# Performance work log

Measured on AMD Instinct MI355X. Metric: run time of the kernel, lower is better.

Reference implementation:

```python
import jax, jax.numpy as jnp
import numpy as np

B, S, D, H = 2, 2048, 1024, 16
DK = D // H

def setup_inputs() -> dict:
    key = jax.random.key(0)
    ks = jax.random.split(key, 5)
    scale = 1.0 / np.sqrt(D)
    return {
        "x": jax.random.normal(ks[0], (B, S, D), dtype=jnp.float32),
        "W_qkv": jax.random.uniform(ks[1], (D, 3 * D), dtype=jnp.float32, minval=-scale, maxval=scale),
        "b_qkv": jax.random.uniform(ks[2], (3 * D,), dtype=jnp.float32, minval=-scale, maxval=scale),
        "W_o": jax.random.uniform(ks[3], (D, D), dtype=jnp.float32, minval=-scale, maxval=scale),
        "b_o": jax.random.uniform(ks[4], (D,), dtype=jnp.float32, minval=-scale, maxval=scale),
    }

def reference(x, W_qkv, b_qkv, W_o, b_o):
    # fused QKV projection: [B,S,3D] -> [B,S,H,3*dk]
    qkv = (x @ W_qkv + b_qkv).reshape(B, S, H, 3 * DK)
    q, k, v = qkv[..., :DK], qkv[..., DK:2 * DK], qkv[..., 2 * DK:]
    # scores [B,H,S,S]; note: original module's masked_fill is a discarded no-op, so no mask applied
    a = jnp.einsum("bqhd,bkhd->bhqk", q, k) / np.sqrt(DK).astype(np.float32)
    a = jax.nn.softmax(a, axis=-1)
    o = jnp.einsum("bhqk,bkhd->bqhd", a, v).reshape(B, S, D)
    return o @ W_o + b_o
```

## Files before the change

kernel.cpp:

```cpp
#include <hip/hip_runtime.h>
#include <hip/hip_bf16.h>

typedef __bf16 bf16;
typedef __attribute__((ext_vector_type(8))) __bf16 bf16x8;
typedef __attribute__((ext_vector_type(4))) __bf16 bf16x4;
typedef __attribute__((ext_vector_type(4))) float f32x4;
typedef __attribute__((ext_vector_type(16))) float f32x16;
typedef __attribute__((ext_vector_type(4))) unsigned int u32x4;
typedef __attribute__((ext_vector_type(2))) unsigned int u32x2;

#define DEV static __device__ __forceinline__

DEV f32x4 mfma16(bf16x8 a, bf16x8 b, f32x4 c) {
  return __builtin_amdgcn_mfma_f32_16x16x32_bf16(a, b, c, 0, 0, 0);
}
DEV f32x16 mfma32(bf16x8 a, bf16x8 b, f32x16 c) {
  return __builtin_amdgcn_mfma_f32_32x32x16_bf16(a, b, c, 0, 0, 0);
}
DEV unsigned int pk2(float a, float b) {
  unsigned short ua = __builtin_bit_cast(unsigned short, (bf16)a);
  unsigned short ub = __builtin_bit_cast(unsigned short, (bf16)b);
  return ((unsigned int)ub << 16) | ua;
}
DEV void gload16(const void* g, void* l) {
  __builtin_amdgcn_global_load_lds(
      (const __attribute__((address_space(1))) unsigned int*)g,
      (__attribute__((address_space(3))) unsigned int*)l, 16, 0, 0);
}
DEV u32x2 xhalf(unsigned int a, unsigned int b, int hi) {
#if __has_builtin(__builtin_amdgcn_permlane32_swap)
  return __builtin_amdgcn_permlane32_swap(a, b, false, false);
#else
  unsigned int xa = __shfl_xor(a, 32), xb = __shfl_xor(b, 32);
  u32x2 r;
  r.x = hi ? xb : a;
  r.y = hi ? b : xa;
  return r;
#endif
}


__global__ __launch_bounds__(256) void xbf_k(const float* __restrict__ x,
                                             bf16* __restrict__ xb) {
  int gid = blockIdx.x * 256 + threadIdx.x;
  const float* src = x + (size_t)gid * 8;
  f32x4 a0 = *(const f32x4*)src;
  f32x4 a1 = *(const f32x4*)(src + 4);
  bf16x8 pk;
#pragma unroll
  for (int j = 0; j < 4; ++j) { pk[j] = (bf16)a0[j]; pk[j + 4] = (bf16)a1[j]; }
  *(bf16x8*)(xb + (size_t)gid * 8) = pk;
}

__global__ __launch_bounds__(256) void wt_k(const float* __restrict__ w,
                                            bf16* __restrict__ wt, int N, int K) {
  __shared__ bf16 ts[64][68];
  const int tid = threadIdx.x;
  const int n0 = blockIdx.x * 64, k0 = blockIdx.y * 64;
  const int tr = tid >> 4;
  const int tc = (tid & 15) * 4;
#pragma unroll
  for (int p = 0; p < 4; ++p) {
    int kr = p * 16 + tr;
    f32x4 v = *(const f32x4*)(w + (size_t)(k0 + kr) * N + n0 + tc);
#pragma unroll
    for (int j = 0; j < 4; ++j) ts[tc + j][kr] = (bf16)v[j];
  }
  __syncthreads();
#pragma unroll
  for (int p = 0; p < 4; ++p) {
    int nr = p * 16 + tr;
    bf16x4 o4;
#pragma unroll
    for (int j = 0; j < 4; ++j) o4[j] = ts[nr][tc + j];
    *(bf16x4*)(wt + (size_t)(n0 + nr) * K + k0 + tc) = o4;
  }
}

__global__ __launch_bounds__(256, 2) void qkv_gemm_k(
    const bf16* __restrict__ xb, const bf16* __restrict__ wt,
    const float* __restrict__ bias,
    bf16* __restrict__ qo, bf16* __restrict__ ko, bf16* __restrict__ vt) {
  __shared__ __align__(16) char As[16384];
  __shared__ __align__(16) char Bs[16384];
  const int tid = threadIdx.x;
  const int lane = tid & 63;
  const int wid = tid >> 6;
  const int wm = wid >> 1, wn = wid & 1;
  const int l16 = lane & 15, lhi = lane >> 4;
  const int m0 = blockIdx.y * 128;
  const int n0 = blockIdx.x * 128;
  const char* ap = (const char*)xb;
  const char* bp = (const char*)wt;

  f32x4 acc[4][4] = {};

  for (int kt = 0; kt < 1024; kt += 64) {
#pragma unroll
    for (int i = 0; i < 4; ++i) {
      int n = i * 256 + wid * 64 + lane;
      int row = n >> 3, c16 = n & 7;
      gload16(ap + (size_t)(m0 + row) * 2048 + kt * 2 + ((c16 * 16) ^ ((row & 7) << 4)),
              As + (i * 256 + wid * 64) * 16);
    }
#pragma unroll
    for (int i = 0; i < 4; ++i) {
      int n = i * 256 + wid * 64 + lane;
      int row = n >> 3, c16 = n & 7;
      gload16(bp + (size_t)(n0 + row) * 2048 + kt * 2 + ((c16 * 16) ^ ((row & 7) << 4)),
              Bs + (i * 256 + wid * 64) * 16);
    }
    __syncthreads();
#pragma unroll
    for (int kc = 0; kc < 2; ++kc) {
      bf16x8 af[4], bfr[4];
#pragma unroll
      for (int ii = 0; ii < 4; ++ii) {
        int row = wm * 64 + ii * 16 + l16;
        af[ii] = *(const bf16x8*)(As + row * 128 +
                                  ((kc * 64 + lhi * 16) ^ ((row & 7) << 4)));
      }
#pragma unroll
      for (int jj = 0; jj < 4; ++jj) {
        int n = wn * 64 + jj * 16 + l16;
        bfr[jj] = *(const bf16x8*)(Bs + n * 128 +
                                   ((kc * 64 + lhi * 16) ^ ((n & 7) << 4)));
      }
#pragma unroll
      for (int ii = 0; ii < 4; ++ii)
#pragma unroll
        for (int jj = 0; jj < 4; ++jj)
          acc[ii][jj] = mfma16(af[ii], bfr[jj], acc[ii][jj]);
    }
    __syncthreads();
  }

  const float SCQ = 0.18033688011112042f;
#pragma unroll
  for (int jj = 0; jj < 4; ++jj) {
    int nbase = n0 + wn * 64 + jj * 16;
    int h = nbase / 192;
    int rem = nbase - h * 192;
    int type = rem >> 6;
    int dk0 = rem & 63;
    float bv = bias[nbase + l16];
    if (type < 2) {
      bf16* dst = (type == 0) ? qo : ko;
      float scl = (type == 0) ? SCQ : 1.0f;
#pragma unroll
      for (int ii = 0; ii < 4; ++ii) {
#pragma unroll
        for (int r = 0; r < 4; ++r) {
          int mrow = m0 + wm * 64 + ii * 16 + lhi * 4 + r;
          int b = mrow >> 11, s = mrow & 2047;
          dst[(size_t)((b * 16 + h) * 2048 + s) * 64 + dk0 + l16] =
              (bf16)((acc[ii][jj][r] + bv) * scl);
        }
      }
    } else {
#pragma unroll
      for (int ii = 0; ii < 4; ++ii) {
        int s0 = m0 + wm * 64 + ii * 16 + lhi * 4;
        int b = s0 >> 11, s = s0 & 2047;
        bf16x4 w4;
#pragma unroll
        for (int r = 0; r < 4; ++r) w4[r] = (bf16)(acc[ii][jj][r] + bv);
        *(bf16x4*)(vt + (size_t)((b * 16 + h) * 64 + dk0 + l16) * 2048 + s) = w4;
      }
    }
  }
}

__global__ __launch_bounds__(256, 4) void attn_k(
    const bf16* __restrict__ q, const bf16* __restrict__ k,
    const bf16* __restrict__ vt, float* __restrict__ opart,
    float* __restrict__ lpart) {
  __shared__ __align__(16) char Ks[2][8192];
  __shared__ __align__(16) char Vs[2][8192];
  const int tid = threadIdx.x;
  const int lane = tid & 63;
  const int wid = tid >> 6;
  const int l31 = lane & 31;
  const int hi = lane >> 5;
  const int bh = blockIdx.x;
  const int half = blockIdx.z;
  const bf16* qp = q + (size_t)bh * 2048 * 64;
  const char* kp = (const char*)(k + (size_t)bh * 2048 * 64);
  const char* vp = (const char*)(vt + (size_t)bh * 64 * 2048);
  const int q0 = blockIdx.y * 128 + wid * 32;
  const int kv0 = half * 1024;

  bf16x8 qf[4];
#pragma unroll
  for (int c = 0; c < 4; ++c)
    qf[c] = *(const bf16x8*)(qp + (size_t)(q0 + l31) * 64 + c * 16 + 8 * hi);

  f32x16 ot0 = {}, ot1 = {};
  float l_ = 0.f;

  auto STAGE = [&](int kt, int bs) {
#pragma unroll
    for (int i = 0; i < 2; ++i) {
      int n = i * 256 + wid * 64 + lane;
      int row = n >> 3, c16 = n & 7;
      const char* src = kp + (size_t)(kt + row) * 128 + ((c16 * 16) ^ ((row & 7) << 4));
      gload16(src, Ks[bs] + (i * 256 + wid * 64) * 16);
    }
#pragma unroll
    for (int i = 0; i < 2; ++i) {
      int n = i * 256 + wid * 64 + lane;
      int row = n >> 3, c16 = n & 7;
      const char* src = vp + (size_t)row * 4096 + (size_t)kt * 2 +
                        ((c16 * 16) ^ ((row & 7) << 4));
      gload16(src, Vs[bs] + (i * 256 + wid * 64) * 16);
    }
  };

  STAGE(kv0, 0);
  __syncthreads();

  for (int t = 0; t < 16; ++t) {
    int bs = t & 1;
    if (t < 15) STAGE(kv0 + (t + 1) * 64, bs ^ 1);

    float p[2][16];
#pragma unroll
    for (int kb = 0; kb < 2; ++kb) {
      bf16x8 kf[4];
#pragma unroll
      for (int c = 0; c < 4; ++c) {
        int row = kb * 32 + l31;
        kf[c] = *(const bf16x8*)(Ks[bs] + row * 128 +
                                 ((c * 32 + 16 * hi) ^ ((row & 7) << 4)));
      }
      f32x16 st = {};
      __builtin_amdgcn_s_setprio(1);
#pragma unroll
      for (int c = 0; c < 4; ++c) st = mfma32(kf[c], qf[c], st);
      __builtin_amdgcn_s_setprio(0);
#pragma unroll
      for (int r = 0; r < 16; ++r) {
        p[kb][r] = __builtin_amdgcn_exp2f(st[r]);
        l_ += p[kb][r];
      }
    }

#pragma unroll
    for (int ch = 0; ch < 4; ++ch) {
      const int kb = ch >> 1, off = (ch & 1) * 8;
      unsigned int w0 = pk2(p[kb][off + 0], p[kb][off + 1]);
      unsigned int w1 = pk2(p[kb][off + 2], p[kb][off + 3]);
      unsigned int w2 = pk2(p[kb][off + 4], p[kb][off + 5]);
      unsigned int w3 = pk2(p[kb][off + 6], p[kb][off + 7]);
      u32x2 s02 = xhalf(w0, w2, hi);
      u32x2 s13 = xhalf(w1, w3, hi);
      u32x4 ww;
      ww.x = s02.x;
      ww.y = s13.x;
      ww.z = s02.y;
      ww.w = s13.y;
      bf16x8 pb = __builtin_bit_cast(bf16x8, ww);
      int r0 = l31, r1 = 32 + l31;
      bf16x8 vf0 = *(const bf16x8*)(Vs[bs] + r0 * 128 +
                                    ((ch * 32 + 16 * hi) ^ ((r0 & 7) << 4)));
      bf16x8 vf1 = *(const bf16x8*)(Vs[bs] + r1 * 128 +
                                    ((ch * 32 + 16 * hi) ^ ((r1 & 7) << 4)));
      __builtin_amdgcn_s_setprio(1);
      ot0 = mfma32(vf0, pb, ot0);
      ot1 = mfma32(vf1, pb, ot1);
      __builtin_amdgcn_s_setprio(0);
    }
    __syncthreads();
  }

  float ltot = l_ + __shfl_xor(l_, 32);
  if (hi == 0) lpart[(size_t)(half * 32 + bh) * 2048 + q0 + l31] = ltot;

  float* op = opart + ((size_t)(half * 32 + bh) * 2048 + q0 + l31) * 64;
#pragma unroll
  for (int g = 0; g < 4; ++g) {
    f32x4 a4, b4;
#pragma unroll
    for (int j = 0; j < 4; ++j) { a4[j] = ot0[g * 4 + j]; b4[j] = ot1[g * 4 + j]; }
    *(f32x4*)(op + 8 * g + 4 * hi) = a4;
    *(f32x4*)(op + 32 + 8 * g + 4 * hi) = b4;
  }
}

__global__ __launch_bounds__(256) void comb_k(const float* __restrict__ opart,
                                              const float* __restrict__ lpart,
                                              bf16* __restrict__ o) {
  const size_t HS = 32ull * 2048 * 64;
  int gid = blockIdx.x * 256 + threadIdx.x;
  int dq = gid & 15;
  int s = (gid >> 4) & 2047;
  int bh = gid >> 15;
  size_t i0 = ((size_t)bh * 2048 + s) * 64 + dq * 4;
  f32x4 a = *(const f32x4*)(opart + i0);
  f32x4 b2 = *(const f32x4*)(opart + HS + i0);
  float l0 = lpart[(size_t)bh * 2048 + s];
  float l1 = lpart[32ull * 2048 + (size_t)bh * 2048 + s];
  float inv = 1.f / (l0 + l1);
  int b = bh >> 4, h = bh & 15;
  bf16x4 r;
#pragma unroll
  for (int j = 0; j < 4; ++j) r[j] = (bf16)((a[j] + b2[j]) * inv);
  *(bf16x4*)(o + (size_t)(b * 2048 + s) * 1024 + h * 64 + dq * 4) = r;
}

__global__ __launch_bounds__(256, 2) void out_gemm_k(
    const bf16* __restrict__ a, const bf16* __restrict__ wt,
    const float* __restrict__ bias, float* __restrict__ out) {
  __shared__ __align__(16) char As[16384];
  __shared__ __align__(16) char Bs[16384];
  const int tid = threadIdx.x;
  const int lane = tid & 63;
  const int wid = tid >> 6;
  const int wm = wid >> 1, wn = wid & 1;
  const int l16 = lane & 15, lhi = lane >> 4;
  const int m0 = blockIdx.y * 128;
  const int n0 = blockIdx.x * 128;
  const char* ap = (const char*)a;
  const char* bp = (const char*)wt;

  f32x4 acc[4][4] = {};

  for (int kt = 0; kt < 1024; kt += 64) {
#pragma unroll
    for (int i = 0; i < 4; ++i) {
      int n = i * 256 + wid * 64 + lane;
      int row = n >> 3, c16 = n & 7;
      gload16(ap + (size_t)(m0 + row) * 2048 + kt * 2 + ((c16 * 16) ^ ((row & 7) << 4)),
              As + (i * 256 + wid * 64) * 16);
    }
#pragma unroll
    for (int i = 0; i < 4; ++i) {
      int n = i * 256 + wid * 64 + lane;
      int row = n >> 3, c16 = n & 7;
      gload16(bp + (size_t)(n0 + row) * 2048 + kt * 2 + ((c16 * 16) ^ ((row & 7) << 4)),
              Bs + (i * 256 + wid * 64) * 16);
    }
    __syncthreads();
#pragma unroll
    for (int kc = 0; kc < 2; ++kc) {
      bf16x8 af[4], bfr[4];
#pragma unroll
      for (int ii = 0; ii < 4; ++ii) {
        int row = wm * 64 + ii * 16 + l16;
        af[ii] = *(const bf16x8*)(As + row * 128 +
                                  ((kc * 64 + lhi * 16) ^ ((row & 7) << 4)));
      }
#pragma unroll
      for (int jj = 0; jj < 4; ++jj) {
        int n = wn * 64 + jj * 16 + l16;
        bfr[jj] = *(const bf16x8*)(Bs + n * 128 +
                                   ((kc * 64 + lhi * 16) ^ ((n & 7) << 4)));
      }
#pragma unroll
      for (int ii = 0; ii < 4; ++ii)
#pragma unroll
        for (int jj = 0; jj < 4; ++jj)
          acc[ii][jj] = mfma16(af[ii], bfr[jj], acc[ii][jj]);
    }
    __syncthreads();
  }

#pragma unroll
  for (int jj = 0; jj < 4; ++jj) {
    int nbase = n0 + wn * 64 + jj * 16;
    float bv = bias[nbase + l16];
#pragma unroll
    for (int ii = 0; ii < 4; ++ii) {
#pragma unroll
      for (int r = 0; r < 4; ++r) {
        int mrow = m0 + wm * 64 + ii * 16 + lhi * 4 + r;
        out[(size_t)mrow * 1024 + nbase + l16] = acc[ii][jj][r] + bv;
      }
    }
  }
}

extern "C" void kernel_launch(void* const* d_in, const int* in_sizes, int n_in,
                              void* d_out, int out_size, void* d_ws, size_t ws_size,
                              hipStream_t stream) {
  const float* x = (const float*)d_in[0];
  const float* wqkv = (const float*)d_in[1];
  const float* bqkv = (const float*)d_in[2];
  const float* wo = (const float*)d_in[3];
  const float* bo = (const float*)d_in[4];
  float* out = (float*)d_out;

  bf16* qws = (bf16*)d_ws;
  bf16* kws = qws + 4194304;
  bf16* vtws = kws + 4194304;
  bf16* ows = vtws + 4194304;
  bf16* wqkvT = ows + 4194304;
  bf16* woT = wqkvT + 3145728;
  float* opart = (float*)(woT + 1048576);
  float* lpart = opart + 8388608;
  bf16* xbf = (bf16*)opart;

  xbf_k<<<2048, 256, 0, stream>>>(x, xbf);
  wt_k<<<dim3(48, 16), 256, 0, stream>>>(wqkv, wqkvT, 3072, 1024);
  wt_k<<<dim3(16, 16), 256, 0, stream>>>(wo, woT, 1024, 1024);
  qkv_gemm_k<<<dim3(24, 32), 256, 0, stream>>>(xbf, wqkvT, bqkv, qws, kws, vtws);
  attn_k<<<dim3(32, 16, 2), 256, 0, stream>>>(qws, kws, vtws, opart, lpart);
  comb_k<<<4096, 256, 0, stream>>>(opart, lpart, ows);
  out_gemm_k<<<dim3(8, 32), 256, 0, stream>>>(ows, woT, bo, out);
}
```

Before: 129.2 us.

## Double query rows per attention wave and merge prep kernels into one launch

Each attention wave now handles 64 query rows instead of 32, so every K/V fragment read from LDS feeds twice as many MFMAs. The grid shrinks to 512 blocks and launch bounds drop to 2 blocks per SIMD group to make room for the larger register footprint. Separately, the x bf16 conversion and the two weight transposes are folded into a single launch to save launch overhead. The cost is fewer resident waves and fewer blocks, which reduces latency hiding and parallelism on a 256-CU device.

```diff
diff --git a/kernel.cpp b/kernel.cpp
--- a/kernel.cpp
+++ b/kernel.cpp
@@ -40,23 +40,36 @@
 }
 
 
-__global__ __launch_bounds__(256) void xbf_k(const float* __restrict__ x,
-                                             bf16* __restrict__ xb) {
-  int gid = blockIdx.x * 256 + threadIdx.x;
-  const float* src = x + (size_t)gid * 8;
-  f32x4 a0 = *(const f32x4*)src;
-  f32x4 a1 = *(const f32x4*)(src + 4);
-  bf16x8 pk;
-#pragma unroll
-  for (int j = 0; j < 4; ++j) { pk[j] = (bf16)a0[j]; pk[j + 4] = (bf16)a1[j]; }
-  *(bf16x8*)(xb + (size_t)gid * 8) = pk;
-}
-
-__global__ __launch_bounds__(256) void wt_k(const float* __restrict__ w,
-                                            bf16* __restrict__ wt, int N, int K) {
+__global__ __launch_bounds__(256) void prep_k(
+    const float* __restrict__ x, bf16* __restrict__ xb,
+    const float* __restrict__ wqkv, bf16* __restrict__ wqkvT,
+    const float* __restrict__ wo, bf16* __restrict__ woT) {
   __shared__ bf16 ts[64][68];
   const int tid = threadIdx.x;
-  const int n0 = blockIdx.x * 64, k0 = blockIdx.y * 64;
+  const int bid = blockIdx.x;
+  if (bid < 2048) {
+    int gid = bid * 256 + tid;
+    const float* src = x + (size_t)gid * 8;
+    f32x4 a0 = *(const f32x4*)src;
+    f32x4 a1 = *(const f32x4*)(src + 4);
+    bf16x8 pk;
+#pragma unroll
+    for (int j = 0; j < 4; ++j) { pk[j] = (bf16)a0[j]; pk[j + 4] = (bf16)a1[j]; }
+    *(bf16x8*)(xb + (size_t)gid * 8) = pk;
+    return;
+  }
+  const float* w;
+  bf16* wt;
+  int N, K, n0, k0;
+  if (bid < 2816) {
+    int r = bid - 2048;
+    w = wqkv; wt = wqkvT; N = 3072; K = 1024;
+    n0 = (r % 48) * 64; k0 = (r / 48) * 64;
+  } else {
+    int r = bid - 2816;
+    w = wo; wt = woT; N = 1024; K = 1024;
+    n0 = (r % 16) * 64; k0 = (r / 16) * 64;
+  }
   const int tr = tid >> 4;
   const int tc = (tid & 15) * 4;
 #pragma unroll
@@ -171,7 +184,7 @@
   }
 }
 
-__global__ __launch_bounds__(256, 4) void attn_k(
+__global__ __launch_bounds__(256, 2) void attn_k(
     const bf16* __restrict__ q, const bf16* __restrict__ k,
     const bf16* __restrict__ vt, float* __restrict__ opart,
     float* __restrict__ lpart) {
@@ -187,16 +200,18 @@
   const bf16* qp = q + (size_t)bh * 2048 * 64;
   const char* kp = (const char*)(k + (size_t)bh * 2048 * 64);
   const char* vp = (const char*)(vt + (size_t)bh * 64 * 2048);
-  const int q0 = blockIdx.y * 128 + wid * 32;
+  const int q0 = blockIdx.y * 256 + wid * 64;
   const int kv0 = half * 1024;
 
-  bf16x8 qf[4];
-#pragma unroll
-  for (int c = 0; c < 4; ++c)
-    qf[c] = *(const bf16x8*)(qp + (size_t)(q0 + l31) * 64 + c * 16 + 8 * hi);
-
-  f32x16 ot0 = {}, ot1 = {};
-  float l_ = 0.f;
+  bf16x8 qf0[4], qf1[4];
+#pragma unroll
+  for (int c = 0; c < 4; ++c) {
+    qf0[c] = *(const bf16x8*)(qp + (size_t)(q0 + l31) * 64 + c * 16 + 8 * hi);
+    qf1[c] = *(const bf16x8*)(qp + (size_t)(q0 + 32 + l31) * 64 + c * 16 + 8 * hi);
+  }
+
+  f32x16 ot00 = {}, ot01 = {}, ot10 = {}, ot11 = {};
+  float l0 = 0.f, l1 = 0.f;
 
   auto STAGE = [&](int kt, int bs) {
 #pragma unroll
@@ -223,7 +238,6 @@
     int bs = t & 1;
     if (t < 15) STAGE(kv0 + (t + 1) * 64, bs ^ 1);
 
-    float p[2][16];
 #pragma unroll
     for (int kb = 0; kb < 2; ++kb) {
       bf16x8 kf[4];
@@ -233,57 +247,83 @@
         kf[c] = *(const bf16x8*)(Ks[bs] + row * 128 +
                                  ((c * 32 + 16 * hi) ^ ((row & 7) << 4)));
       }
-      f32x16 st = {};
+      f32x16 st0 = {}, st1 = {};
       __builtin_amdgcn_s_setprio(1);
 #pragma unroll
-      for (int c = 0; c < 4; ++c) st = mfma32(kf[c], qf[c], st);
+      for (int c = 0; c < 4; ++c) {
+        st0 = mfma32(kf[c], qf0[c], st0);
+        st1 = mfma32(kf[c], qf1[c], st1);
+      }
       __builtin_amdgcn_s_setprio(0);
+      float p0[16], p1[16];
 #pragma unroll
       for (int r = 0; r < 16; ++r) {
-        p[kb][r] = __builtin_amdgcn_exp2f(st[r]);
-        l_ += p[kb][r];
-      }
-    }
-
-#pragma unroll
-    for (int ch = 0; ch < 4; ++ch) {
-      const int kb = ch >> 1, off = (ch & 1) * 8;
-      unsigned int w0 = pk2(p[kb][off + 0], p[kb][off + 1]);
-      unsigned int w1 = pk2(p[kb][off + 2], p[kb][off + 3]);
-      unsigned int w2 = pk2(p[kb][off + 4], p[kb][off + 5]);
-      unsigned int w3 = pk2(p[kb][off + 6], p[kb][off + 7]);
-      u32x2 s02 = xhalf(w0, w2, hi);
-      u32x2 s13 = xhalf(w1, w3, hi);
-      u32x4 ww;
-      ww.x = s02.x;
-      ww.y = s13.x;
-      ww.z = s02.y;
-      ww.w = s13.y;
-      bf16x8 pb = __builtin_bit_cast(bf16x8, ww);
-      int r0 = l31, r1 = 32 + l31;
-      bf16x8 vf0 = *(const bf16x8*)(Vs[bs] + r0 * 128 +
-                                    ((ch * 32 + 16 * hi) ^ ((r0 & 7) << 4)));
-      bf16x8 vf1 = *(const bf16x8*)(Vs[bs] + r1 * 128 +
-                                    ((ch * 32 + 16 * hi) ^ ((r1 & 7) << 4)));
-      __builtin_amdgcn_s_setprio(1);
-      ot0 = mfma32(vf0, pb, ot0);
-      ot1 = mfma32(vf1, pb, ot1);
-      __builtin_amdgcn_s_setprio(0);
+        p0[r] = __builtin_amdgcn_exp2f(st0[r]);
+        l0 += p0[r];
+        p1[r] = __builtin_amdgcn_exp2f(st1[r]);
+        l1 += p1[r];
+      }
+
+#pragma unroll
+      for (int c2 = 0; c2 < 2; ++c2) {
+        const int off = c2 * 8;
+        unsigned int a0 = pk2(p0[off + 0], p0[off + 1]);
+        unsigned int a1 = pk2(p0[off + 2], p0[off + 3]);
+        unsigned int a2 = pk2(p0[off + 4], p0[off + 5]);
+        unsigned int a3 = pk2(p0[off + 6], p0[off + 7]);
+        u32x2 s02 = xhalf(a0, a2, hi);
+        u32x2 s13 = xhalf(a1, a3, hi);
+        u32x4 wwa;
+        wwa.x = s02.x; wwa.y = s13.x; wwa.z = s02.y; wwa.w = s13.y;
+        bf16x8 pb0 = __builtin_bit_cast(bf16x8, wwa);
+        unsigned int b0 = pk2(p1[off + 0], p1[off + 1]);
+        unsigned int b1 = pk2(p1[off + 2], p1[off + 3]);
+        unsigned int b2 = pk2(p1[off + 4], p1[off + 5]);
+        unsigned int b3 = pk2(p1[off + 6], p1[off + 7]);
+        u32x2 t02 = xhalf(b0, b2, hi);
+        u32x2 t13 = xhalf(b1, b3, hi);
+        u32x4 wwb;
+        wwb.x = t02.x; wwb.y = t13.x; wwb.z = t02.y; wwb.w = t13.y;
+        bf16x8 pb1 = __builtin_bit_cast(bf16x8, wwb);
+
+        int col = kb * 64 + c2 * 32 + 16 * hi;
+        int r0 = l31, r1 = 32 + l31;
+        bf16x8 vf0 = *(const bf16x8*)(Vs[bs] + r0 * 128 + (col ^ ((r0 & 7) << 4)));
+        bf16x8 vf1 = *(const bf16x8*)(Vs[bs] + r1 * 128 + (col ^ ((r1 & 7) << 4)));
+        __builtin_amdgcn_s_setprio(1);
+        ot00 = mfma32(vf0, pb0, ot00);
+        ot01 = mfma32(vf1, pb0, ot01);
+        ot10 = mfma32(vf0, pb1, ot10);
+        ot11 = mfma32(vf1, pb1, ot11);
+        __builtin_amdgcn_s_setprio(0);
+      }
     }
     __syncthreads();
   }
 
-  float ltot = l_ + __shfl_xor(l_, 32);
-  if (hi == 0) lpart[(size_t)(half * 32 + bh) * 2048 + q0 + l31] = ltot;
-
-  float* op = opart + ((size_t)(half * 32 + bh) * 2048 + q0 + l31) * 64;
+  float lt0 = l0 + __shfl_xor(l0, 32);
+  float lt1 = l1 + __shfl_xor(l1, 32);
+  if (hi == 0) {
+    lpart[(size_t)(half * 32 + bh) * 2048 + q0 + l31] = lt0;
+    lpart[(size_t)(half * 32 + bh) * 2048 + q0 + 32 + l31] = lt1;
+  }
+
+  float* op0 = opart + ((size_t)(half * 32 + bh) * 2048 + q0 + l31) * 64;
+  float* op1 = opart + ((size_t)(half * 32 + bh) * 2048 + q0 + 32 + l31) * 64;
 #pragma unroll
   for (int g = 0; g < 4; ++g) {
-    f32x4 a4, b4;
-#pragma unroll
-    for (int j = 0; j < 4; ++j) { a4[j] = ot0[g * 4 + j]; b4[j] = ot1[g * 4 + j]; }
-    *(f32x4*)(op + 8 * g + 4 * hi) = a4;
-    *(f32x4*)(op + 32 + 8 * g + 4 * hi) = b4;
+    f32x4 a4, b4, c4, d4;
+#pragma unroll
+    for (int j = 0; j < 4; ++j) {
+      a4[j] = ot00[g * 4 + j];
+      b4[j] = ot01[g * 4 + j];
+      c4[j] = ot10[g * 4 + j];
+      d4[j] = ot11[g * 4 + j];
+    }
+    *(f32x4*)(op0 + 8 * g + 4 * hi) = a4;
+    *(f32x4*)(op0 + 32 + 8 * g + 4 * hi) = b4;
+    *(f32x4*)(op1 + 8 * g + 4 * hi) = c4;
+    *(f32x4*)(op1 + 32 + 8 * g + 4 * hi) = d4;
   }
 }
 
@@ -400,11 +440,9 @@
   float* lpart = opart + 8388608;
   bf16* xbf = (bf16*)opart;
 
-  xbf_k<<<2048, 256, 0, stream>>>(x, xbf);
-  wt_k<<<dim3(48, 16), 256, 0, stream>>>(wqkv, wqkvT, 3072, 1024);
-  wt_k<<<dim3(16, 16), 256, 0, stream>>>(wo, woT, 1024, 1024);
+  prep_k<<<3072, 256, 0, stream>>>(x, xbf, wqkv, wqkvT, wo, woT);
   qkv_gemm_k<<<dim3(24, 32), 256, 0, stream>>>(xbf, wqkvT, bqkv, qws, kws, vtws);
-  attn_k<<<dim3(32, 16, 2), 256, 0, stream>>>(qws, kws, vtws, opart, lpart);
+  attn_k<<<dim3(32, 8, 2), 256, 0, stream>>>(qws, kws, vtws, opart, lpart);
   comb_k<<<4096, 256, 0, stream>>>(opart, lpart, ows);
   out_gemm_k<<<dim3(8, 32), 256, 0, stream>>>(ows, woT, bo, out);
 }
```

New measurement: 127.7 us. About the same (-1.1%).
